# Performance work log

Measured on AMD Instinct MI355X. Metric: run time of the kernel, lower is better.

Reference implementation:

```python
import jax, jax.numpy as jnp
import numpy as np


def setup_inputs() -> dict:
    key = jax.random.key(0)
    k1, k2, k3 = jax.random.split(key, 3)
    B, N, C = 4, 1024, 768
    x = jax.random.normal(k1, (B, N, C), dtype=jnp.float32)
    w_qkv = jax.random.normal(k2, (C, 3 * C), dtype=jnp.float32) * 0.02
    b_qkv = jnp.zeros((3 * C,), dtype=jnp.float32)
    w_proj = jax.random.normal(k3, (C, C), dtype=jnp.float32) * 0.02
    b_proj = jnp.zeros((C,), dtype=jnp.float32)
    return {"x": x, "w_qkv": w_qkv, "b_qkv": b_qkv,
            "w_proj": w_proj, "b_proj": b_proj, "num_heads": 12}


def reference(x, w_qkv, b_qkv, w_proj, b_proj, num_heads):
    B, N, C = x.shape
    h = num_heads
    d = C // h
    qkv = x @ w_qkv + b_qkv                       # (B, N, 3C)
    # einops '(h d qkv)': qkv index is innermost -> reshape to (B,N,h,d,3)
    qkv = qkv.reshape(B, N, h, d, 3)
    qkv = jnp.transpose(qkv, (4, 0, 2, 1, 3))     # (3, B, h, N, d)
    q, k, v = qkv[0], qkv[1], qkv[2]
    scaling = jnp.sqrt(jnp.asarray(C, dtype=x.dtype))  # NOTE: sqrt(embed_size), per source
    attn = jnp.einsum('bhqd,bhkd->bhqk', q, k) / scaling
    attn = jax.nn.softmax(attn, axis=-1)
    out = jnp.einsum('bhqk,bhkd->bhqd', attn, v)  # (B, h, N, d)
    out = jnp.transpose(out, (0, 2, 1, 3)).reshape(B, N, C)
    return out @ w_proj + b_proj
```

## Files before the change

kernel.cpp:

```cpp
#include <hip/hip_runtime.h>
#include <cstdint>

typedef __attribute__((ext_vector_type(8))) short short8;
typedef __attribute__((ext_vector_type(4))) short short4v;
typedef __attribute__((ext_vector_type(4))) float f32x4;
typedef unsigned short ushort_t;

#define MFMA(a, b, c) __builtin_amdgcn_mfma_f32_16x16x32_bf16(a, b, c, 0, 0, 0)

__device__ __forceinline__ ushort_t f2bf(float f) {
    unsigned u = __float_as_uint(f);
    u += 0x7FFF + ((u >> 16) & 1);
    return (ushort_t)(u >> 16);
}

__device__ __forceinline__ void gld_lds16(const ushort_t* g, ushort_t* l) {
    __builtin_amdgcn_global_load_lds(
        (__attribute__((address_space(1))) void*)g,
        (__attribute__((address_space(3))) void*)l, 16, 0, 0);
}

__global__ __launch_bounds__(256) void cvt_bf(const float* __restrict__ in,
                                              ushort_t* __restrict__ out, int n) {
    int i = (blockIdx.x * 256 + threadIdx.x) * 8;
    if (i >= n) return;
    float4 a = *(const float4*)&in[i];
    float4 b = *(const float4*)&in[i + 4];
    uint4 v;
    v.x = f2bf(a.x) | (f2bf(a.y) << 16);
    v.y = f2bf(a.z) | (f2bf(a.w) << 16);
    v.z = f2bf(b.x) | (f2bf(b.y) << 16);
    v.w = f2bf(b.z) | (f2bf(b.w) << 16);
    *(uint4*)&out[i] = v;
}

__global__ __launch_bounds__(256) void wtrans(const float* __restrict__ w,
                                              ushort_t* __restrict__ out,
                                              int K, int J, int mode, float scale) {
    __shared__ float t[64][68];
    const int k0 = blockIdx.y * 64, j0 = blockIdx.x * 64;
    for (int g = threadIdx.x; g < 1024; g += 256) {
        int r = g >> 4, c4 = g & 15;
        float4 v = *(const float4*)&w[(size_t)(k0 + r) * J + j0 + c4 * 4];
        *(float4*)&t[r][c4 * 4] = v;
    }
    __syncthreads();
    const int jj = threadIdx.x >> 2, kc = threadIdx.x & 3;
    const int j = j0 + jj;
    int jp; float s;
    if (mode == 0) {
        int which = j % 3, hh = j / 192, d = (j % 192) / 3;
        jp = which * 768 + hh * 64 + d;
        s = (which == 0) ? scale : 1.f;
    } else { jp = j; s = 1.f; }
    ushort_t o[16];
    #pragma unroll
    for (int i = 0; i < 16; ++i) o[i] = f2bf(t[kc * 16 + i][jj] * s);
    uint4 v0, v1;
    v0.x = o[0] | (o[1] << 16);  v0.y = o[2] | (o[3] << 16);
    v0.z = o[4] | (o[5] << 16);  v0.w = o[6] | (o[7] << 16);
    v1.x = o[8] | (o[9] << 16);  v1.y = o[10] | (o[11] << 16);
    v1.z = o[12] | (o[13] << 16); v1.w = o[14] | (o[15] << 16);
    *(uint4*)&out[(size_t)jp * K + k0 + kc * 16] = v0;
    *(uint4*)&out[(size_t)jp * K + k0 + kc * 16 + 8] = v1;
}

__global__ void bias_perm(const float* __restrict__ bq, float* __restrict__ out,
                          float scale) {
    int j = blockIdx.x * 256 + threadIdx.x;
    if (j < 2304) {
        int which = j % 3, hh = j / 192, d = (j % 192) / 3;
        out[which * 768 + hh * 64 + d] = bq[j] * (which == 0 ? scale : 1.f);
    }
}

__global__ __launch_bounds__(256) void vtrans(const ushort_t* __restrict__ qkv,
                                              ushort_t* __restrict__ Vt) {
    __shared__ ushort_t t[64][72];
    const int bh = blockIdx.y, b = bh / 12, h = bh % 12;
    const int n0 = blockIdx.x * 64;
    for (int g = threadIdx.x; g < 512; g += 256) {
        int r = g >> 3, c8 = g & 7;
        uint4 v = *(const uint4*)&qkv[(size_t)(b * 1024 + n0 + r) * 2304 + 1536 + h * 64 + c8 * 8];
        *(uint4*)&t[r][c8 * 8] = v;
    }
    __syncthreads();
    for (int g = threadIdx.x; g < 512; g += 256) {
        int d = g >> 3, n8 = g & 7;
        ushort_t o[8];
        #pragma unroll
        for (int i = 0; i < 8; ++i) o[i] = t[n8 * 8 + i][d];
        uint4 v;
        v.x = o[0] | (o[1] << 16); v.y = o[2] | (o[3] << 16);
        v.z = o[4] | (o[5] << 16); v.w = o[6] | (o[7] << 16);
        *(uint4*)&Vt[(size_t)bh * 65536 + (size_t)d * 1024 + n0 + n8 * 8] = v;
    }
}

template <int OUT_BF16>
__global__ __launch_bounds__(256, 2) void gemm_mfma(
    const ushort_t* __restrict__ A, const ushort_t* __restrict__ Bt,
    const float* __restrict__ bias, void* __restrict__ Cout,
    int M, int N, int K) {
    __shared__ ushort_t As[128 * 64];
    __shared__ ushort_t Bs[128 * 64];

    const int tid = threadIdx.x;
    const int lane = tid & 63;
    const int wv = tid >> 6;
    const int wr = wv >> 1, wc = wv & 1;
    const int l15 = lane & 15;
    const int lg = lane >> 4;

    const int m0 = blockIdx.y * 128;
    const int n0 = blockIdx.x * 128;

    const int rbase = tid >> 3;
    const int c8l = tid & 7;
    const int swz8 = (c8l ^ (rbase & 7)) * 8;

    const ushort_t* gA = A + (size_t)(m0 + rbase) * K + swz8;
    const ushort_t* gB = Bt + (size_t)(n0 + rbase) * K + swz8;
    ushort_t* lA = As + tid * 8;
    ushort_t* lB = Bs + tid * 8;

    f32x4 acc[4][4];
    #pragma unroll
    for (int i = 0; i < 4; ++i)
        #pragma unroll
        for (int j = 0; j < 4; ++j) acc[i][j] = (f32x4){0.f, 0.f, 0.f, 0.f};

    for (int k0 = 0; k0 < K; k0 += 64) {
        #pragma unroll
        for (int rr = 0; rr < 4; ++rr) {
            gld_lds16(gA + (size_t)rr * 32 * K + k0, lA + rr * 2048);
            gld_lds16(gB + (size_t)rr * 32 * K + k0, lB + rr * 2048);
        }
        __syncthreads();

        #pragma unroll
        for (int kk = 0; kk < 2; ++kk) {
            short8 af[4], bfr[4];
            #pragma unroll
            for (int mt = 0; mt < 4; ++mt) {
                int row = wr * 64 + mt * 16 + l15;
                int gr = (kk * 4 + lg) ^ (row & 7);
                af[mt] = *(const short8*)&As[row * 64 + gr * 8];
            }
            #pragma unroll
            for (int nt = 0; nt < 4; ++nt) {
                int row = wc * 64 + nt * 16 + l15;
                int gr = (kk * 4 + lg) ^ (row & 7);
                bfr[nt] = *(const short8*)&Bs[row * 64 + gr * 8];
            }
            #pragma unroll
            for (int mt = 0; mt < 4; ++mt)
                #pragma unroll
                for (int nt = 0; nt < 4; ++nt)
                    acc[mt][nt] = MFMA(af[mt], bfr[nt], acc[mt][nt]);
        }
        __syncthreads();
    }

    #pragma unroll
    for (int nt = 0; nt < 4; ++nt) {
        int col = n0 + wc * 64 + nt * 16 + l15;
        float bb = bias[col];
        #pragma unroll
        for (int mt = 0; mt < 4; ++mt) {
            int row = m0 + wr * 64 + mt * 16 + lg * 4;
            #pragma unroll
            for (int r = 0; r < 4; ++r) {
                float v = acc[mt][nt][r] + bb;
                if (OUT_BF16)
                    ((ushort_t*)Cout)[(size_t)(row + r) * N + col] = f2bf(v);
                else
                    ((float*)Cout)[(size_t)(row + r) * N + col] = v;
            }
        }
    }
}

__global__ __launch_bounds__(256, 2) void attn_mfma(
    const ushort_t* __restrict__ qkv,
    const ushort_t* __restrict__ Vt,
    ushort_t* __restrict__ outp) {
    __shared__ ushort_t Qs[64 * 64];
    __shared__ ushort_t Ks[64 * 64];
    __shared__ ushort_t Vs[64 * 64];
    __shared__ ushort_t Ps[4][16 * 64];

    const int tid = threadIdx.x;
    const int lane = tid & 63;
    const int wv = tid >> 6;
    const int l15 = lane & 15;
    const int lg = lane >> 4;

    const int bh = blockIdx.y;
    const int b = bh / 12, h = bh % 12;
    const int q0 = blockIdx.x * 64;

    const int rbase = tid >> 3;
    const int c8l = tid & 7;
    const int swz8 = (c8l ^ (rbase & 7)) * 8;

    const ushort_t* gQ = qkv + (size_t)(b * 1024 + q0 + rbase) * 2304 + h * 64 + swz8;
    const ushort_t* gK = qkv + (size_t)(b * 1024 + rbase) * 2304 + 768 + h * 64 + swz8;
    const ushort_t* gV = Vt + (size_t)bh * 65536 + (size_t)rbase * 1024 + swz8;

    gld_lds16(gQ, Qs + tid * 8);
    gld_lds16(gQ + (size_t)32 * 2304, Qs + tid * 8 + 2048);
    __syncthreads();

    short8 bq[2];
    {
        int row = wv * 16 + l15;
        #pragma unroll
        for (int kk = 0; kk < 2; ++kk) {
            int gr = (kk * 4 + lg) ^ (row & 7);
            bq[kk] = *(const short8*)&Qs[row * 64 + gr * 8];
        }
    }

    float m_run = -1e30f, l_run = 0.f;
    f32x4 o[4];
    #pragma unroll
    for (int dt = 0; dt < 4; ++dt) o[dt] = (f32x4){0.f, 0.f, 0.f, 0.f};

    for (int kt = 0; kt < 16; ++kt) {
        gld_lds16(gK + (size_t)(kt * 64) * 2304, Ks + tid * 8);
        gld_lds16(gK + (size_t)(kt * 64 + 32) * 2304, Ks + tid * 8 + 2048);
        gld_lds16(gV + kt * 64, Vs + tid * 8);
        gld_lds16(gV + kt * 64 + 32 * 1024, Vs + tid * 8 + 2048);
        __syncthreads();

        f32x4 s[4];
        #pragma unroll
        for (int st = 0; st < 4; ++st) {
            int row = st * 16 + l15;
            int g0 = (0 + lg) ^ (row & 7);
            int g1 = (4 + lg) ^ (row & 7);
            short8 a0 = *(const short8*)&Ks[row * 64 + g0 * 8];
            short8 a1 = *(const short8*)&Ks[row * 64 + g1 * 8];
            f32x4 z = (f32x4){0.f, 0.f, 0.f, 0.f};
            z = MFMA(a0, bq[0], z);
            z = MFMA(a1, bq[1], z);
            s[st] = z;
        }

        float mloc = -1e30f;
        #pragma unroll
        for (int st = 0; st < 4; ++st)
            #pragma unroll
            for (int r = 0; r < 4; ++r) mloc = fmaxf(mloc, s[st][r]);
        mloc = fmaxf(mloc, __shfl_xor(mloc, 16));
        mloc = fmaxf(mloc, __shfl_xor(mloc, 32));
        float mnew = fmaxf(m_run, mloc);
        float corr = __expf(m_run - mnew);
        float psum = 0.f;
        #pragma unroll
        for (int st = 0; st < 4; ++st)
            #pragma unroll
            for (int r = 0; r < 4; ++r) {
                float p = __expf(s[st][r] - mnew);
                s[st][r] = p;
                psum += p;
            }
        psum += __shfl_xor(psum, 16);
        psum += __shfl_xor(psum, 32);
        l_run = l_run * corr + psum;
        m_run = mnew;
        #pragma unroll
        for (int dt = 0; dt < 4; ++dt)
            #pragma unroll
            for (int r = 0; r < 4; ++r) o[dt][r] *= corr;

        ushort_t* pb = Ps[wv];
        #pragma unroll
        for (int st = 0; st < 4; ++st) {
            int g8 = st * 2 + (lg >> 1);
            int byteoff = l15 * 128 + ((g8 ^ (l15 & 7)) * 16) + (lg & 1) * 8;
            short4v pv = {(short)f2bf(s[st][0]), (short)f2bf(s[st][1]),
                          (short)f2bf(s[st][2]), (short)f2bf(s[st][3])};
            *(short4v*)((char*)pb + byteoff) = pv;
        }

        #pragma unroll
        for (int kk = 0; kk < 2; ++kk) {
            int grp = (kk * 4 + lg) ^ (l15 & 7);
            short8 bp = *(const short8*)&pb[l15 * 64 + grp * 8];
            #pragma unroll
            for (int dt = 0; dt < 4; ++dt) {
                int row = dt * 16 + l15;
                int ga = (kk * 4 + lg) ^ (row & 7);
                short8 av = *(const short8*)&Vs[row * 64 + ga * 8];
                o[dt] = MFMA(av, bp, o[dt]);
            }
        }
        __syncthreads();
    }

    const float inv = 1.f / l_run;
    const int qrow = b * 1024 + q0 + wv * 16 + l15;
    #pragma unroll
    for (int dt = 0; dt < 4; ++dt)
        #pragma unroll
        for (int r = 0; r < 4; ++r) {
            int d = dt * 16 + lg * 4 + r;
            outp[(size_t)qrow * 768 + h * 64 + d] = f2bf(o[dt][r] * inv);
        }
}

extern "C" void kernel_launch(void* const* d_in, const int* in_sizes, int n_in,
                              void* d_out, int out_size, void* d_ws, size_t ws_size,
                              hipStream_t stream) {
    const float* x = (const float*)d_in[0];
    const float* w_qkv = (const float*)d_in[1];
    const float* b_qkv = (const float*)d_in[2];
    const float* w_proj = (const float*)d_in[3];
    const float* b_proj = (const float*)d_in[4];
    float* outp = (float*)d_out;

    char* ws = (char*)d_ws;
    ushort_t* x_bf = (ushort_t*)ws;   ws += (size_t)4096 * 768 * 2;
    ushort_t* wqT = (ushort_t*)ws;    ws += (size_t)2304 * 768 * 2;
    ushort_t* wpT = (ushort_t*)ws;    ws += (size_t)768 * 768 * 2;
    float* bq_p = (float*)ws;         ws += (size_t)2304 * 4;
    ushort_t* qkv_bf = (ushort_t*)ws; ws += (size_t)4096 * 2304 * 2;
    ushort_t* Vt = (ushort_t*)ws;     ws += (size_t)48 * 64 * 1024 * 2;
    ushort_t* aout = (ushort_t*)ws;

    const float scale = 0.036084391824351615f;

    cvt_bf<<<(4096 * 768) / (256 * 8), 256, 0, stream>>>(x, x_bf, 4096 * 768);
    wtrans<<<dim3(2304 / 64, 768 / 64), 256, 0, stream>>>(w_qkv, wqT, 768, 2304, 0, scale);
    wtrans<<<dim3(768 / 64, 768 / 64), 256, 0, stream>>>(w_proj, wpT, 768, 768, 1, 1.f);
    bias_perm<<<9, 256, 0, stream>>>(b_qkv, bq_p, scale);

    gemm_mfma<1><<<dim3(2304 / 128, 4096 / 128), 256, 0, stream>>>(
        x_bf, wqT, bq_p, qkv_bf, 4096, 2304, 768);

    vtrans<<<dim3(16, 48), 256, 0, stream>>>(qkv_bf, Vt);

    attn_mfma<<<dim3(16, 48), 256, 0, stream>>>(qkv_bf, Vt, aout);

    gemm_mfma<0><<<dim3(768 / 128, 4096 / 128), 256, 0, stream>>>(
        aout, wpT, b_proj, outp, 4096, 768, 768);
}
```

Before: 95.64 us.

## Fuse prep kernels, double-buffer GEMM and attention, widen attention query tile

After: 105.3 us. 1.1x slower.

```diff
diff --git a/kernel.cpp b/kernel.cpp
--- a/kernel.cpp
+++ b/kernel.cpp
@@ -20,57 +20,69 @@
         (__attribute__((address_space(3))) void*)l, 16, 0, 0);
 }
 
-__global__ __launch_bounds__(256) void cvt_bf(const float* __restrict__ in,
-                                              ushort_t* __restrict__ out, int n) {
-    int i = (blockIdx.x * 256 + threadIdx.x) * 8;
-    if (i >= n) return;
-    float4 a = *(const float4*)&in[i];
-    float4 b = *(const float4*)&in[i + 4];
-    uint4 v;
-    v.x = f2bf(a.x) | (f2bf(a.y) << 16);
-    v.y = f2bf(a.z) | (f2bf(a.w) << 16);
-    v.z = f2bf(b.x) | (f2bf(b.y) << 16);
-    v.w = f2bf(b.z) | (f2bf(b.w) << 16);
-    *(uint4*)&out[i] = v;
-}
-
-__global__ __launch_bounds__(256) void wtrans(const float* __restrict__ w,
-                                              ushort_t* __restrict__ out,
-                                              int K, int J, int mode, float scale) {
+__global__ __launch_bounds__(256) void prep(
+    const float* __restrict__ x, ushort_t* __restrict__ x_bf,
+    const float* __restrict__ w_qkv, ushort_t* __restrict__ wqT,
+    const float* __restrict__ w_proj, ushort_t* __restrict__ wpT,
+    const float* __restrict__ b_qkv, float* __restrict__ bq_p, float scale) {
     __shared__ float t[64][68];
-    const int k0 = blockIdx.y * 64, j0 = blockIdx.x * 64;
-    for (int g = threadIdx.x; g < 1024; g += 256) {
-        int r = g >> 4, c4 = g & 15;
-        float4 v = *(const float4*)&w[(size_t)(k0 + r) * J + j0 + c4 * 4];
-        *(float4*)&t[r][c4 * 4] = v;
-    }
-    __syncthreads();
-    const int jj = threadIdx.x >> 2, kc = threadIdx.x & 3;
-    const int j = j0 + jj;
-    int jp; float s;
-    if (mode == 0) {
-        int which = j % 3, hh = j / 192, d = (j % 192) / 3;
-        jp = which * 768 + hh * 64 + d;
-        s = (which == 0) ? scale : 1.f;
-    } else { jp = j; s = 1.f; }
-    ushort_t o[16];
-    #pragma unroll
-    for (int i = 0; i < 16; ++i) o[i] = f2bf(t[kc * 16 + i][jj] * s);
-    uint4 v0, v1;
-    v0.x = o[0] | (o[1] << 16);  v0.y = o[2] | (o[3] << 16);
-    v0.z = o[4] | (o[5] << 16);  v0.w = o[6] | (o[7] << 16);
-    v1.x = o[8] | (o[9] << 16);  v1.y = o[10] | (o[11] << 16);
-    v1.z = o[12] | (o[13] << 16); v1.w = o[14] | (o[15] << 16);
-    *(uint4*)&out[(size_t)jp * K + k0 + kc * 16] = v0;
-    *(uint4*)&out[(size_t)jp * K + k0 + kc * 16 + 8] = v1;
-}
-
-__global__ void bias_perm(const float* __restrict__ bq, float* __restrict__ out,
-                          float scale) {
-    int j = blockIdx.x * 256 + threadIdx.x;
-    if (j < 2304) {
-        int which = j % 3, hh = j / 192, d = (j % 192) / 3;
-        out[which * 768 + hh * 64 + d] = bq[j] * (which == 0 ? scale : 1.f);
+    const int bid = blockIdx.x;
+    const int tid = threadIdx.x;
+
+    if (bid < 1536) {
+        int i = (bid * 256 + tid) * 8;
+        float4 a = *(const float4*)&x[i];
+        float4 b = *(const float4*)&x[i + 4];
+        uint4 v;
+        v.x = f2bf(a.x) | (f2bf(a.y) << 16);
+        v.y = f2bf(a.z) | (f2bf(a.w) << 16);
+        v.z = f2bf(b.x) | (f2bf(b.y) << 16);
+        v.w = f2bf(b.z) | (f2bf(b.w) << 16);
+        *(uint4*)&x_bf[i] = v;
+        return;
+    }
+    if (bid < 2112) {
+        const int qkv_mode = bid < 1968;
+        const int local = qkv_mode ? bid - 1536 : bid - 1968;
+        const int nbx = qkv_mode ? 36 : 12;
+        const int J = qkv_mode ? 2304 : 768;
+        const float* w = qkv_mode ? w_qkv : w_proj;
+        ushort_t* out = qkv_mode ? wqT : wpT;
+        const int j0 = (local % nbx) * 64;
+        const int k0 = (local / nbx) * 64;
+        const int K = 768;
+        for (int g = tid; g < 1024; g += 256) {
+            int r = g >> 4, c4 = g & 15;
+            float4 v = *(const float4*)&w[(size_t)(k0 + r) * J + j0 + c4 * 4];
+            *(float4*)&t[r][c4 * 4] = v;
+        }
+        __syncthreads();
+        const int jj = tid >> 2, kc = tid & 3;
+        const int j = j0 + jj;
+        int jp; float s;
+        if (qkv_mode) {
+            int which = j % 3, hh = j / 192, d = (j % 192) / 3;
+            jp = which * 768 + hh * 64 + d;
+            s = (which == 0) ? scale : 1.f;
+        } else { jp = j; s = 1.f; }
+        ushort_t o[16];
+        #pragma unroll
+        for (int i = 0; i < 16; ++i) o[i] = f2bf(t[kc * 16 + i][jj] * s);
+        uint4 v0, v1;
+        v0.x = o[0] | (o[1] << 16);  v0.y = o[2] | (o[3] << 16);
+        v0.z = o[4] | (o[5] << 16);  v0.w = o[6] | (o[7] << 16);
+        v1.x = o[8] | (o[9] << 16);  v1.y = o[10] | (o[11] << 16);
+        v1.z = o[12] | (o[13] << 16); v1.w = o[14] | (o[15] << 16);
+        *(uint4*)&out[(size_t)jp * K + k0 + kc * 16] = v0;
+        *(uint4*)&out[(size_t)jp * K + k0 + kc * 16 + 8] = v1;
+        return;
+    }
+    {
+        int j = (bid - 2112) * 256 + tid;
+        if (j < 2304) {
+            int which = j % 3, hh = j / 192, d = (j % 192) / 3;
+            bq_p[which * 768 + hh * 64 + d] = b_qkv[j] * (which == 0 ? scale : 1.f);
+        }
     }
 }
 
@@ -102,8 +114,8 @@
     const ushort_t* __restrict__ A, const ushort_t* __restrict__ Bt,
     const float* __restrict__ bias, void* __restrict__ Cout,
     int M, int N, int K) {
-    __shared__ ushort_t As[128 * 64];
-    __shared__ ushort_t Bs[128 * 64];
+    __shared__ ushort_t As[2 * 8192];
+    __shared__ ushort_t Bs[2 * 8192];
 
     const int tid = threadIdx.x;
     const int lane = tid & 63;
@@ -121,8 +133,16 @@
 
     const ushort_t* gA = A + (size_t)(m0 + rbase) * K + swz8;
     const ushort_t* gB = Bt + (size_t)(n0 + rbase) * K + swz8;
-    ushort_t* lA = As + tid * 8;
-    ushort_t* lB = Bs + tid * 8;
+
+    auto stage = [&](int buf, int k0) {
+        ushort_t* la = As + buf * 8192 + tid * 8;
+        ushort_t* lb = Bs + buf * 8192 + tid * 8;
+        #pragma unroll
+        for (int rr = 0; rr < 4; ++rr) {
+            gld_lds16(gA + (size_t)rr * 32 * K + k0, la + rr * 2048);
+            gld_lds16(gB + (size_t)rr * 32 * K + k0, lb + rr * 2048);
+        }
+    };
 
     f32x4 acc[4][4];
     #pragma unroll
@@ -130,14 +150,15 @@
         #pragma unroll
         for (int j = 0; j < 4; ++j) acc[i][j] = (f32x4){0.f, 0.f, 0.f, 0.f};
 
-    for (int k0 = 0; k0 < K; k0 += 64) {
-        #pragma unroll
-        for (int rr = 0; rr < 4; ++rr) {
-            gld_lds16(gA + (size_t)rr * 32 * K + k0, lA + rr * 2048);
-            gld_lds16(gB + (size_t)rr * 32 * K + k0, lB + rr * 2048);
-        }
-        __syncthreads();
-
+    const int nk = K >> 6;
+    stage(0, 0);
+    __syncthreads();
+
+    int cur = 0;
+    for (int t = 0; t < nk; ++t) {
+        if (t + 1 < nk) stage(cur ^ 1, (t + 1) * 64);
+        const ushort_t* as = As + cur * 8192;
+        const ushort_t* bs = Bs + cur * 8192;
         #pragma unroll
         for (int kk = 0; kk < 2; ++kk) {
             short8 af[4], bfr[4];
@@ -145,13 +166,13 @@
             for (int mt = 0; mt < 4; ++mt) {
                 int row = wr * 64 + mt * 16 + l15;
                 int gr = (kk * 4 + lg) ^ (row & 7);
-                af[mt] = *(const short8*)&As[row * 64 + gr * 8];
+                af[mt] = *(const short8*)&as[row * 64 + gr * 8];
             }
             #pragma unroll
             for (int nt = 0; nt < 4; ++nt) {
                 int row = wc * 64 + nt * 16 + l15;
                 int gr = (kk * 4 + lg) ^ (row & 7);
-                bfr[nt] = *(const short8*)&Bs[row * 64 + gr * 8];
+                bfr[nt] = *(const short8*)&bs[row * 64 + gr * 8];
             }
             #pragma unroll
             for (int mt = 0; mt < 4; ++mt)
@@ -160,6 +181,7 @@
                     acc[mt][nt] = MFMA(af[mt], bfr[nt], acc[mt][nt]);
         }
         __syncthreads();
+        cur ^= 1;
     }
 
     #pragma unroll
@@ -185,10 +207,10 @@
     const ushort_t* __restrict__ qkv,
     const ushort_t* __restrict__ Vt,
     ushort_t* __restrict__ outp) {
-    __shared__ ushort_t Qs[64 * 64];
-    __shared__ ushort_t Ks[64 * 64];
-    __shared__ ushort_t Vs[64 * 64];
-    __shared__ ushort_t Ps[4][16 * 64];
+    __shared__ ushort_t Qs[128 * 64];
+    __shared__ ushort_t Ks[2 * 4096];
+    __shared__ ushort_t Vs[2 * 4096];
+    __shared__ ushort_t Ps[4 * 2048];
 
     const int tid = threadIdx.x;
     const int lane = tid & 63;
@@ -198,7 +220,7 @@
 
     const int bh = blockIdx.y;
     const int b = bh / 12, h = bh % 12;
-    const int q0 = blockIdx.x * 64;
+    const int q0 = blockIdx.x * 128;
 
     const int rbase = tid >> 3;
     const int c8l = tid & 7;
@@ -208,107 +230,145 @@
     const ushort_t* gK = qkv + (size_t)(b * 1024 + rbase) * 2304 + 768 + h * 64 + swz8;
     const ushort_t* gV = Vt + (size_t)bh * 65536 + (size_t)rbase * 1024 + swz8;
 
-    gld_lds16(gQ, Qs + tid * 8);
-    gld_lds16(gQ + (size_t)32 * 2304, Qs + tid * 8 + 2048);
+    auto stageKV = [&](int buf, int kt) {
+        gld_lds16(gK + (size_t)(kt * 64) * 2304, Ks + buf * 4096 + tid * 8);
+        gld_lds16(gK + (size_t)(kt * 64 + 32) * 2304, Ks + buf * 4096 + 2048 + tid * 8);
+        gld_lds16(gV + kt * 64, Vs + buf * 4096 + tid * 8);
+        gld_lds16(gV + kt * 64 + 32 * 1024, Vs + buf * 4096 + 2048 + tid * 8);
+    };
+
+    #pragma unroll
+    for (int c = 0; c < 4; ++c)
+        gld_lds16(gQ + (size_t)(c * 32) * 2304, Qs + c * 2048 + tid * 8);
+    stageKV(0, 0);
     __syncthreads();
 
-    short8 bq[2];
-    {
-        int row = wv * 16 + l15;
+    short8 bq[2][2];
+    #pragma unroll
+    for (int qf = 0; qf < 2; ++qf) {
+        int row = wv * 32 + qf * 16 + l15;
         #pragma unroll
         for (int kk = 0; kk < 2; ++kk) {
             int gr = (kk * 4 + lg) ^ (row & 7);
-            bq[kk] = *(const short8*)&Qs[row * 64 + gr * 8];
-        }
-    }
-
-    float m_run = -1e30f, l_run = 0.f;
-    f32x4 o[4];
-    #pragma unroll
-    for (int dt = 0; dt < 4; ++dt) o[dt] = (f32x4){0.f, 0.f, 0.f, 0.f};
-
+            bq[kk][qf] = *(const short8*)&Qs[row * 64 + gr * 8];
+        }
+    }
+
+    float m_run[2] = {-1e30f, -1e30f};
+    float l_run[2] = {0.f, 0.f};
+    f32x4 o[4][2];
+    #pragma unroll
+    for (int dt = 0; dt < 4; ++dt)
+        #pragma unroll
+        for (int qf = 0; qf < 2; ++qf) o[dt][qf] = (f32x4){0.f, 0.f, 0.f, 0.f};
+
+    int cur = 0;
     for (int kt = 0; kt < 16; ++kt) {
-        gld_lds16(gK + (size_t)(kt * 64) * 2304, Ks + tid * 8);
-        gld_lds16(gK + (size_t)(kt * 64 + 32) * 2304, Ks + tid * 8 + 2048);
-        gld_lds16(gV + kt * 64, Vs + tid * 8);
-        gld_lds16(gV + kt * 64 + 32 * 1024, Vs + tid * 8 + 2048);
-        __syncthreads();
-
-        f32x4 s[4];
+        if (kt < 15) stageKV(cur ^ 1, kt + 1);
+        const ushort_t* ks = Ks + cur * 4096;
+        const ushort_t* vs = Vs + cur * 4096;
+
+        f32x4 s[4][2];
         #pragma unroll
         for (int st = 0; st < 4; ++st) {
             int row = st * 16 + l15;
-            int g0 = (0 + lg) ^ (row & 7);
-            int g1 = (4 + lg) ^ (row & 7);
-            short8 a0 = *(const short8*)&Ks[row * 64 + g0 * 8];
-            short8 a1 = *(const short8*)&Ks[row * 64 + g1 * 8];
-            f32x4 z = (f32x4){0.f, 0.f, 0.f, 0.f};
-            z = MFMA(a0, bq[0], z);
-            z = MFMA(a1, bq[1], z);
-            s[st] = z;
-        }
-
-        float mloc = -1e30f;
-        #pragma unroll
-        for (int st = 0; st < 4; ++st)
-            #pragma unroll
-            for (int r = 0; r < 4; ++r) mloc = fmaxf(mloc, s[st][r]);
-        mloc = fmaxf(mloc, __shfl_xor(mloc, 16));
-        mloc = fmaxf(mloc, __shfl_xor(mloc, 32));
-        float mnew = fmaxf(m_run, mloc);
-        float corr = __expf(m_run - mnew);
-        float psum = 0.f;
-        #pragma unroll
-        for (int st = 0; st < 4; ++st)
-            #pragma unroll
-            for (int r = 0; r < 4; ++r) {
-                float p = __expf(s[st][r] - mnew);
-                s[st][r] = p;
-                psum += p;
-            }
-        psum += __shfl_xor(psum, 16);
-        psum += __shfl_xor(psum, 32);
-        l_run = l_run * corr + psum;
-        m_run = mnew;
-        #pragma unroll
-        for (int dt = 0; dt < 4; ++dt)
-            #pragma unroll
-            for (int r = 0; r < 4; ++r) o[dt][r] *= corr;
-
-        ushort_t* pb = Ps[wv];
-        #pragma unroll
-        for (int st = 0; st < 4; ++st) {
-            int g8 = st * 2 + (lg >> 1);
-            int byteoff = l15 * 128 + ((g8 ^ (l15 & 7)) * 16) + (lg & 1) * 8;
-            short4v pv = {(short)f2bf(s[st][0]), (short)f2bf(s[st][1]),
-                          (short)f2bf(s[st][2]), (short)f2bf(s[st][3])};
-            *(short4v*)((char*)pb + byteoff) = pv;
+            short8 a0 = *(const short8*)&ks[row * 64 + (((0 + lg) ^ (row & 7)) * 8)];
+            short8 a1 = *(const short8*)&ks[row * 64 + (((4 + lg) ^ (row & 7)) * 8)];
+            #pragma unroll
+            for (int qf = 0; qf < 2; ++qf) {
+                f32x4 z = (f32x4){0.f, 0.f, 0.f, 0.f};
+                z = MFMA(a0, bq[0][qf], z);
+                z = MFMA(a1, bq[1][qf], z);
+                s[st][qf] = z;
+            }
+        }
+
+        #pragma unroll
+        for (int qf = 0; qf < 2; ++qf) {
+            float mloc = -1e30f;
+            #pragma unroll
+            for (int st = 0; st < 4; ++st)
+                #pragma unroll
+                for (int r = 0; r < 4; ++r) mloc = fmaxf(mloc, s[st][qf][r]);
+            mloc = fmaxf(mloc, __shfl_xor(mloc, 16));
+            mloc = fmaxf(mloc, __shfl_xor(mloc, 32));
+            float mnew = fmaxf(m_run[qf], mloc);
+            float corr = __expf(m_run[qf] - mnew);
+            float psum = 0.f;
+            #pragma unroll
+            for (int st = 0; st < 4; ++st)
+                #pragma unroll
+                for (int r = 0; r < 4; ++r) {
+                    float p = __expf(s[st][qf][r] - mnew);
+                    s[st][qf][r] = p;
+                    psum += p;
+                }
+            psum += __shfl_xor(psum, 16);
+            psum += __shfl_xor(psum, 32);
+            l_run[qf] = l_run[qf] * corr + psum;
+            m_run[qf] = mnew;
+            #pragma unroll
+            for (int dt = 0; dt < 4; ++dt)
+                #pragma unroll
+                for (int r = 0; r < 4; ++r) o[dt][qf][r] *= corr;
+        }
+
+        ushort_t* pb = Ps + wv * 2048;
+        #pragma unroll
+        for (int qf = 0; qf < 2; ++qf) {
+            int row = qf * 16 + l15;
+            #pragma unroll
+            for (int st = 0; st < 4; ++st) {
+                int g8 = st * 2 + (lg >> 1);
+                int byteoff = row * 128 + ((g8 ^ (row & 7)) * 16) + (lg & 1) * 8;
+                short4v pv = {(short)f2bf(s[st][qf][0]), (short)f2bf(s[st][qf][1]),
+                              (short)f2bf(s[st][qf][2]), (short)f2bf(s[st][qf][3])};
+                *(short4v*)((char*)pb + byteoff) = pv;
+            }
         }
 
         #pragma unroll
         for (int kk = 0; kk < 2; ++kk) {
-            int grp = (kk * 4 + lg) ^ (l15 & 7);
-            short8 bp = *(const short8*)&pb[l15 * 64 + grp * 8];
+            short8 bp[2];
+            #pragma unroll
+            for (int qf = 0; qf < 2; ++qf) {
+                int row = qf * 16 + l15;
+                int grp = (kk * 4 + lg) ^ (row & 7);
+                bp[qf] = *(const short8*)&pb[row * 64 + grp * 8];
+            }
             #pragma unroll
             for (int dt = 0; dt < 4; ++dt) {
                 int row = dt * 16 + l15;
                 int ga = (kk * 4 + lg) ^ (row & 7);
-                short8 av = *(const short8*)&Vs[row * 64 + ga * 8];
-                o[dt] = MFMA(av, bp, o[dt]);
+                short8 av = *(const short8*)&vs[row * 64 + ga * 8];
+                #pragma unroll
+                for (int qf = 0; qf < 2; ++qf)
+                    o[dt][qf] = MFMA(av, bp[qf], o[dt][qf]);
             }
         }
         __syncthreads();
-    }
-
-    const float inv = 1.f / l_run;
-    const int qrow = b * 1024 + q0 + wv * 16 + l15;
-    #pragma unroll
-    for (int dt = 0; dt < 4; ++dt)
-        #pragma unroll
-        for (int r = 0; r < 4; ++r) {
-            int d = dt * 16 + lg * 4 + r;
-            outp[(size_t)qrow * 768 + h * 64 + d] = f2bf(o[dt][r] * inv);
-        }
+        cur ^= 1;
+    }
+
+    float inv[2] = {1.f / l_run[0], 1.f / l_run[1]};
+    ushort_t* pb = Ps + wv * 2048;
+    #pragma unroll
+    for (int qf = 0; qf < 2; ++qf)
+        #pragma unroll
+        for (int dt = 0; dt < 4; ++dt) {
+            short4v pv = {(short)f2bf(o[dt][qf][0] * inv[qf]),
+                          (short)f2bf(o[dt][qf][1] * inv[qf]),
+                          (short)f2bf(o[dt][qf][2] * inv[qf]),
+                          (short)f2bf(o[dt][qf][3] * inv[qf])};
+            *(short4v*)&pb[(qf * 16 + l15) * 64 + dt * 16 + lg * 4] = pv;
+        }
+    #pragma unroll
+    for (int pass = 0; pass < 4; ++pass) {
+        int idx = pass * 64 + lane;
+        int row = idx >> 3, c8 = idx & 7;
+        uint4 v = *(const uint4*)&pb[row * 64 + c8 * 8];
+        *(uint4*)&outp[(size_t)(b * 1024 + q0 + wv * 32 + row) * 768 + h * 64 + c8 * 8] = v;
+    }
 }
 
 extern "C" void kernel_launch(void* const* d_in, const int* in_sizes, int n_in,
@@ -332,18 +392,16 @@
 
     const float scale = 0.036084391824351615f;
 
-    cvt_bf<<<(4096 * 768) / (256 * 8), 256, 0, stream>>>(x, x_bf, 4096 * 768);
-    wtrans<<<dim3(2304 / 64, 768 / 64), 256, 0, stream>>>(w_qkv, wqT, 768, 2304, 0, scale);
-    wtrans<<<dim3(768 / 64, 768 / 64), 256, 0, stream>>>(w_proj, wpT, 768, 768, 1, 1.f);
-    bias_perm<<<9, 256, 0, stream>>>(b_qkv, bq_p, scale);
-
-    gemm_mfma<1><<<dim3(2304 / 128, 4096 / 128), 256, 0, stream>>>(
+    prep<<<2121, 256, 0, stream>>>(x, x_bf, w_qkv, wqT, w_proj, wpT,
+                                   b_qkv, bq_p, scale);
+
+    gemm_mfma<1><<<dim3(18, 32), 256, 0, stream>>>(
         x_bf, wqT, bq_p, qkv_bf, 4096, 2304, 768);
 
     vtrans<<<dim3(16, 48), 256, 0, stream>>>(qkv_bf, Vt);
 
-    attn_mfma<<<dim3(16, 48), 256, 0, stream>>>(qkv_bf, Vt, aout);
-
-    gemm_mfma<0><<<dim3(768 / 128, 4096 / 128), 256, 0, stream>>>(
+    attn_mfma<<<dim3(8, 48), 256, 0, stream>>>(qkv_bf, Vt, aout);
+
+    gemm_mfma<0><<<dim3(6, 32), 256, 0, stream>>>(
         aout, wpT, b_proj, outp, 4096, 768, 768);
 }
```
